# Kernel optimization log

Measured on AMD Instinct MI355X. Metric: run time of the kernel, lower is better.

Reference implementation:

```python
import jax, jax.numpy as jnp
import numpy as np

B, S, E, CS, NC, H = 4, 2048, 1024, 16, 8, 16
D = E + CS            # d_model = 1040
DH = D // H           # head_dim = 65
DFF = 4 * E           # forward_expansion * embed_size


def setup_inputs() -> dict:
    key = jax.random.key(0)
    ks = jax.random.split(key, 20)
    s = 0.02  # init scale for weights
    f32 = jnp.float32
    return {
        'x': jax.random.normal(ks[0], (B, S, E), f32),
        'conditioning': jax.random.uniform(ks[1], (B, S, CS), f32),
        # attention params (torch Linear convention: W is [out, in])
        'Wq': jax.random.normal(ks[2], (D, D), f32) * s,
        'bq': jnp.zeros((D,), f32),
        'Wv': jax.random.normal(ks[3], (D, D), f32) * s,
        'bv': jnp.zeros((D,), f32),
        'Wk': jax.random.normal(ks[4], (NC, D, D), f32) * s,  # stacked per-class key projections
        'bk': jnp.zeros((NC, D), f32),
        'Wo': jax.random.normal(ks[5], (D, D), f32) * s,
        'bo': jnp.zeros((D,), f32),
        # layernorms
        'g1': jnp.ones((E,), f32), 'bn1': jnp.zeros((E,), f32),
        'g2': jnp.ones((E,), f32), 'bn2': jnp.zeros((E,), f32),
        # feed-forward
        'Wf1': jax.random.normal(ks[6], (DFF, E), f32) * s,
        'bf1': jnp.zeros((DFF,), f32),
        'Wf2': jax.random.normal(ks[7], (E, DFF), f32) * s,
        'bf2': jnp.zeros((E,), f32),
    }


def _layernorm(x, g, b, eps=1e-5):
    m = jnp.mean(x, axis=-1, keepdims=True)
    v = jnp.mean(jnp.square(x - m), axis=-1, keepdims=True)
    return (x - m) * jax.lax.rsqrt(v + eps) * g + b


def reference(x, conditioning, Wq, bq, Wv, bv, Wk, bk, Wo, bo,
              g1, bn1, g2, bn2, Wf1, bf1, Wf2, bf2):
    # dropout is identity (eval mode)
    xn = _layernorm(x, g1, bn1)                       # [B,S,E]
    xc = jnp.concatenate([xn, conditioning], axis=-1)  # [B,S,D]

    q = (xc @ Wq.T + bq).reshape(B, S, H, DH).transpose(0, 2, 1, 3)  # [B,H,S,DH]
    v = (xc @ Wv.T + bv).reshape(B, S, H, DH).transpose(0, 2, 1, 3)

    # per-class keys: [B,C,S,D], then weighted-sum by conditioning[:,:,:NC]
    keys = jnp.einsum('bsd,cod->bcso', xc, Wk) + bk[None, :, None, :]
    w = conditioning[:, :, :NC]                        # [B,S,C]
    k = jnp.einsum('bsc,bcso->bso', w, keys)           # [B,S,D]
    k = k.reshape(B, S, H, DH).transpose(0, 2, 1, 3)   # [B,H,S,DH]

    scale = 1.0 / np.sqrt(DH).astype(np.float32)
    scores = jnp.einsum('bhqd,bhkd->bhqk', q, k) * scale
    attn = jax.nn.softmax(scores, axis=-1)
    o = jnp.einsum('bhqk,bhkd->bhqd', attn, v)
    o = o.transpose(0, 2, 1, 3).reshape(B, S, D)
    o = o @ Wo.T + bo

    h = xn + o[:, :, :E]                               # residual uses normed x
    ff = jnp.maximum(h @ Wf1.T + bf1, 0.0) @ Wf2.T + bf2
    return _layernorm(h + ff, g2, bn2)
```

## Files before the change

### kernel.cpp

```cpp
#include <hip/hip_runtime.h>
#include <hip/hip_bf16.h>
#include <math.h>

typedef __bf16 bf16;
typedef __bf16 v8bf __attribute__((ext_vector_type(8)));
typedef float v4f __attribute__((ext_vector_type(4)));

#define B_   4
#define S_   2048
#define E_   1024
#define CS_  16
#define NC_  8
#define H_   16
#define D_   1040
#define DH_  65
#define DFF_ 4096
#define M_   8192
#define KC_  1056
#define KH_  (4 * KC_)
#define KB2_ (8 * KC_)

__device__ __forceinline__ v4f mfma16(v8bf a, v8bf b, v4f c) {
    return __builtin_amdgcn_mfma_f32_16x16x32_bf16(a, b, c, 0, 0, 0);
}

__device__ __forceinline__ void async16(const bf16* g, bf16* l) {
    __builtin_amdgcn_global_load_lds(
        (const __attribute__((address_space(1))) unsigned int*)g,
        (__attribute__((address_space(3))) unsigned int*)l, 16, 0, 0);
}

__global__ __launch_bounds__(256) void k_cvt(const float* __restrict__ src,
                                             bf16* __restrict__ dst, int n) {
    int i = (blockIdx.x * 256 + threadIdx.x) * 4;
    if (i + 4 <= n) {
        float4 v = *(const float4*)(src + i);
        bf16 o[4] = {(bf16)v.x, (bf16)v.y, (bf16)v.z, (bf16)v.w};
        *(ushort4*)(dst + i) = *(const ushort4*)o;
    }
}

__global__ __launch_bounds__(256) void k_build_bk(const float* __restrict__ Wk,
                                                  bf16* __restrict__ Bp) {
    int c = blockIdx.y;
    int idx = blockIdx.x * 256 + threadIdx.x;
    if (idx >= 1040 * 130) return;
    int n = idx / 130, u = idx - n * 130;
    const float* src = Wk + ((size_t)(c * D_ + n)) * D_ + u * 8;
    float4 a = *(const float4*)src;
    float4 b = *(const float4*)(src + 4);
    bf16 o[8] = {(bf16)a.x, (bf16)a.y, (bf16)a.z, (bf16)a.w,
                 (bf16)b.x, (bf16)b.y, (bf16)b.z, (bf16)b.w};
    *(uint4*)(Bp + (size_t)n * KB2_ + c * KC_ + u * 8) = *(const uint4*)o;
}

__global__ __launch_bounds__(256) void k_scale_a(const bf16* __restrict__ xc,
                                                 const float* __restrict__ cond,
                                                 int coff, bf16* __restrict__ Ap) {
    int idx = blockIdx.x * 256 + threadIdx.x;
    int m = idx / 132, u = idx - m * 132;
    int j = u * 8;
    float4 w4 = *(const float4*)(cond + (size_t)m * CS_ + coff);
    float wv[4] = {w4.x, w4.y, w4.z, w4.w};
    bf16* dst = Ap + (size_t)m * KH_ + j;
    if (j < D_) {
        union { uint4 u4; bf16 h[8]; } src;
        src.u4 = *(const uint4*)(xc + (size_t)m * D_ + j);
        float xv[8];
#pragma unroll
        for (int e = 0; e < 8; ++e) xv[e] = (float)src.h[e];
#pragma unroll
        for (int cc = 0; cc < 4; ++cc) {
            bf16 o[8];
#pragma unroll
            for (int e = 0; e < 8; ++e) o[e] = (bf16)(xv[e] * wv[cc]);
            *(uint4*)(dst + cc * KC_) = *(const uint4*)o;
        }
    } else {
        uint4 z = {0u, 0u, 0u, 0u};
#pragma unroll
        for (int cc = 0; cc < 4; ++cc) *(uint4*)(dst + cc * KC_) = z;
    }
}

__global__ __launch_bounds__(256) void k_zero_pads(bf16* __restrict__ qp,
                                                   bf16* __restrict__ kp) {
    int i = blockIdx.x * 256 + threadIdx.x;
    int row = i >> 3, j = i & 7;
    uint4 z = {0u, 0u, 0u, 0u};
    bf16* base = (j < 4) ? qp : kp;
    ((uint4*)(base + (size_t)row * 96 + 64))[j & 3] = z;
}

__global__ __launch_bounds__(256) void k_ln_concat(
    const float* __restrict__ x, const float* __restrict__ cond,
    const float* __restrict__ g, const float* __restrict__ bn,
    bf16* __restrict__ xc)
{
    int row = blockIdx.x;
    int t = threadIdx.x;
    const float* xr = x + (size_t)row * E_;
    float4 v = *(const float4*)(xr + t * 4);
    float s = v.x + v.y + v.z + v.w;
    float ss = v.x * v.x + v.y * v.y + v.z * v.z + v.w * v.w;
#pragma unroll
    for (int off = 32; off; off >>= 1) {
        s  += __shfl_down(s, off);
        ss += __shfl_down(ss, off);
    }
    __shared__ float red[8];
    int wid = t >> 6;
    if ((t & 63) == 0) { red[wid] = s; red[4 + wid] = ss; }
    __syncthreads();
    float stot  = red[0] + red[1] + red[2] + red[3];
    float sstot = red[4] + red[5] + red[6] + red[7];
    float mean = stot * (1.0f / E_);
    float var  = sstot * (1.0f / E_) - mean * mean;
    float rs = rsqrtf(var + 1e-5f);
    bf16* xcr = xc + (size_t)row * D_;
    float vv[4] = {v.x, v.y, v.z, v.w};
#pragma unroll
    for (int j = 0; j < 4; ++j) {
        int i = t * 4 + j;
        xcr[i] = (bf16)(((vv[j] - mean) * rs) * g[i] + bn[i]);
    }
    if (t < CS_) xcr[E_ + t] = (bf16)cond[(size_t)row * CS_ + t];
}

__global__ __launch_bounds__(256) void k_gemm_k2(
    const bf16* __restrict__ A, const bf16* __restrict__ Bm,
    int koffB, bf16* __restrict__ Pout)
{
    __shared__ bf16 As[128][32];
    __shared__ bf16 Bs[128][32];
    int t = threadIdx.x;

    int pid = blockIdx.x;
    int gid = pid / 72;
    int rem = pid - gid * 72;
    int mi = gid * 8 + (rem & 7);
    int ni = rem >> 3;
    int m0 = mi << 7, n0 = ni << 7;

    int lane = t & 63, w = t >> 6;
    int wm = (w >> 1) * 64, wn = (w & 1) * 64;
    int lr = lane & 15, lq = lane >> 4;

    int row_i[2], seg_i[2];
#pragma unroll
    for (int i = 0; i < 2; ++i) { row_i[i] = (t + i * 256) >> 2; seg_i[i] = (t + i * 256) & 3; }

    v4f acc[4][4];
    v4f vzero = {0.f, 0.f, 0.f, 0.f};
#pragma unroll
    for (int mt = 0; mt < 4; ++mt)
#pragma unroll
        for (int nt = 0; nt < 4; ++nt) acc[mt][nt] = vzero;

    for (int kb = 0; kb < KH_ / 32; ++kb) {
        int k0 = kb << 5;
#pragma unroll
        for (int i = 0; i < 2; ++i) {
            async16(A + (size_t)(m0 + row_i[i]) * KH_ + k0 + seg_i[i] * 8,
                    &As[0][0] + (t + i * 256) * 8);
            async16(Bm + (size_t)(n0 + row_i[i]) * KB2_ + koffB + k0 + seg_i[i] * 8,
                    &Bs[0][0] + (t + i * 256) * 8);
        }
        __syncthreads();
        v8bf af[4], bfr[4];
#pragma unroll
        for (int mt = 0; mt < 4; ++mt) af[mt]  = *(const v8bf*)(&As[wm + mt * 16 + lr][lq * 8]);
#pragma unroll
        for (int nt = 0; nt < 4; ++nt) bfr[nt] = *(const v8bf*)(&Bs[wn + nt * 16 + lr][lq * 8]);
#pragma unroll
        for (int mt = 0; mt < 4; ++mt)
#pragma unroll
            for (int nt = 0; nt < 4; ++nt)
                acc[mt][nt] = mfma16(af[mt], bfr[nt], acc[mt][nt]);
        __syncthreads();
    }

#pragma unroll
    for (int mt = 0; mt < 4; ++mt)
#pragma unroll
        for (int reg = 0; reg < 4; ++reg) {
            int grow = m0 + wm + mt * 16 + lq * 4 + reg;
#pragma unroll
            for (int nt = 0; nt < 4; ++nt) {
                int gcol = n0 + wn + nt * 16 + lr;
                if (gcol < D_)
                    Pout[(size_t)grow * D_ + gcol] = (bf16)acc[mt][nt][reg];
            }
        }
}

__global__ __launch_bounds__(256) void k_comb_k(
    const bf16* __restrict__ P0, const bf16* __restrict__ P1,
    const float* __restrict__ condw, const float* __restrict__ bkp,
    bf16* __restrict__ kp)
{
    int idx = blockIdx.x * 256 + threadIdx.x;
    int m = idx / 1040, n = idx - m * 1040;
    float v = (float)P0[idx] + (float)P1[idx];
#pragma unroll
    for (int c = 0; c < NC_; ++c)
        v += condw[(size_t)m * CS_ + c] * bkp[(size_t)c * D_ + n];
    int h = n / 65, d = n - h * 65;
    int b = m >> 11, s = m & 2047;
    int d2 = (d < 64) ? (d ^ ((s & 7) << 3)) : (d ^ ((s & 3) << 3));
    kp[(((size_t)(b * 16 + h)) * S_ + s) * 96 + d2] = (bf16)v;
}

#define EP_QV  0
#define EP_O   1
#define EP_FF1 2
#define EP_FF2 3

template<int EP>
__global__ __launch_bounds__(256) void k_gemm(
    const bf16* __restrict__ A, const bf16* __restrict__ Bm,
    const float* __restrict__ bias, const float* __restrict__ bias2,
    int M, int N, int K, int lda, int ldb, int nbn,
    bf16* __restrict__ Cb, float* __restrict__ Cf, int ldc,
    const bf16* __restrict__ res, int ldres, bf16* __restrict__ Cb2)
{
    __shared__ bf16 As[128][32];
    __shared__ bf16 Bs[128][32];
    int t = threadIdx.x;

    int pid = blockIdx.x;
    int nig = 8 * nbn;
    int gid = pid / nig;
    int rem = pid - gid * nig;
    int mi = gid * 8 + (rem & 7);
    int ni = rem >> 3;
    int m0 = mi << 7, n0 = ni << 7;

    int lane = t & 63, w = t >> 6;
    int wm = (w >> 1) * 64, wn = (w & 1) * 64;
    int lr = lane & 15, lq = lane >> 4;

    int row_i[2], seg_i[2];
#pragma unroll
    for (int i = 0; i < 2; ++i) { row_i[i] = (t + i * 256) >> 2; seg_i[i] = (t + i * 256) & 3; }

    v4f acc[4][4];
    v4f vzero = {0.f, 0.f, 0.f, 0.f};
#pragma unroll
    for (int mt = 0; mt < 4; ++mt)
#pragma unroll
        for (int nt = 0; nt < 4; ++nt) acc[mt][nt] = vzero;

    const int KF = K >> 5;
    const bool KR = (K & 31) != 0;

    for (int kb = 0; kb < KF; ++kb) {
        int k0 = kb << 5;
#pragma unroll
        for (int i = 0; i < 2; ++i) {
            async16(A + (size_t)(m0 + row_i[i]) * lda + k0 + seg_i[i] * 8,
                    &As[0][0] + (t + i * 256) * 8);
            async16(Bm + (size_t)(n0 + row_i[i]) * ldb + k0 + seg_i[i] * 8,
                    &Bs[0][0] + (t + i * 256) * 8);
        }
        __syncthreads();
        v8bf af[4], bfr[4];
#pragma unroll
        for (int mt = 0; mt < 4; ++mt) af[mt]  = *(const v8bf*)(&As[wm + mt * 16 + lr][lq * 8]);
#pragma unroll
        for (int nt = 0; nt < 4; ++nt) bfr[nt] = *(const v8bf*)(&Bs[wn + nt * 16 + lr][lq * 8]);
#pragma unroll
        for (int mt = 0; mt < 4; ++mt)
#pragma unroll
            for (int nt = 0; nt < 4; ++nt)
                acc[mt][nt] = mfma16(af[mt], bfr[nt], acc[mt][nt]);
        __syncthreads();
    }
    if (KR) {
        int k0 = KF << 5;
#pragma unroll
        for (int i = 0; i < 2; ++i) {
            int gk = k0 + seg_i[i] * 8;
            uint4 val = {0u, 0u, 0u, 0u};
            if (gk + 8 <= K) val = *(const uint4*)(A + (size_t)(m0 + row_i[i]) * lda + gk);
            *(uint4*)(&As[row_i[i]][seg_i[i] * 8]) = val;
            uint4 bv = {0u, 0u, 0u, 0u};
            int gn = n0 + row_i[i];
            if (gn < N && gk + 8 <= K) bv = *(const uint4*)(Bm + (size_t)gn * ldb + gk);
            *(uint4*)(&Bs[row_i[i]][seg_i[i] * 8]) = bv;
        }
        __syncthreads();
        v8bf af[4], bfr[4];
#pragma unroll
        for (int mt = 0; mt < 4; ++mt) af[mt]  = *(const v8bf*)(&As[wm + mt * 16 + lr][lq * 8]);
#pragma unroll
        for (int nt = 0; nt < 4; ++nt) bfr[nt] = *(const v8bf*)(&Bs[wn + nt * 16 + lr][lq * 8]);
#pragma unroll
        for (int mt = 0; mt < 4; ++mt)
#pragma unroll
            for (int nt = 0; nt < 4; ++nt)
                acc[mt][nt] = mfma16(af[mt], bfr[nt], acc[mt][nt]);
        __syncthreads();
    }

#pragma unroll
    for (int mt = 0; mt < 4; ++mt) {
#pragma unroll
        for (int reg = 0; reg < 4; ++reg) {
            int grow = m0 + wm + mt * 16 + lq * 4 + reg;
#pragma unroll
            for (int nt = 0; nt < 4; ++nt) {
                int gcol = n0 + wn + nt * 16 + lr;
                float vacc = acc[mt][nt][reg];
                if constexpr (EP == EP_QV) {
                    if (gcol < D_) {
                        float o = (vacc + bias[gcol]) * 0.1789442960f;
                        int h = gcol / 65, d = gcol - h * 65;
                        int b = grow >> 11, s = grow & 2047;
                        Cb[(((size_t)(b * 16 + h)) * S_ + s) * 96 + d] = (bf16)o;
                    } else if (gcol < 2 * D_) {
                        int col = gcol - D_;
                        Cb2[(size_t)grow * D_ + col] = (bf16)(vacc + bias2[col]);
                    }
                } else if constexpr (EP == EP_O) {
                    float o = vacc + bias[gcol] + (float)res[(size_t)grow * ldres + gcol];
                    Cb[(size_t)grow * ldc + gcol] = (bf16)o;
                } else if constexpr (EP == EP_FF1) {
                    float o = vacc + bias[gcol];
                    Cb[(size_t)grow * ldc + gcol] = (bf16)fmaxf(o, 0.f);
                } else {
                    Cf[(size_t)grow * ldc + gcol] =
                        vacc + bias[gcol] + (float)res[(size_t)grow * ldres + gcol];
                }
            }
        }
    }
}

__global__ __launch_bounds__(256) void k_transpose_v(
    const bf16* __restrict__ v, bf16* __restrict__ vt)
{
    int bh = blockIdx.y, s0 = blockIdx.x * 64;
    int b = bh >> 4, h = bh & 15;
    __shared__ bf16 tile[80][65];
#pragma unroll
    for (int i = 0; i < 20; ++i) {
        int idx = threadIdx.x + i * 256;
        int d = idx % 80, sl = idx / 80;
        bf16 val = (bf16)0.f;
        if (d < DH_) val = v[((size_t)b * S_ + s0 + sl) * D_ + h * DH_ + d];
        tile[d][sl] = val;
    }
    __syncthreads();
#pragma unroll
    for (int i = 0; i < 20; ++i) {
        int idx = threadIdx.x + i * 256;
        int sl = idx % 64, d = idx / 64;
        int sl2 = sl ^ ((d & 7) << 3);
        vt[((size_t)bh * 80 + d) * S_ + s0 + sl2] = tile[d][sl];
    }
}

__global__ __launch_bounds__(256) void k_attn(
    const bf16* __restrict__ qp, const bf16* __restrict__ kp,
    const bf16* __restrict__ vt, bf16* __restrict__ o)
{
    int bh = blockIdx.y;
    int s0 = blockIdx.x * 128;
    int b = bh >> 4, h = bh & 15;
    int t = threadIdx.x, lane = t & 63, w = t >> 6;
    int lr = lane & 15, lq = lane >> 4;

    __shared__ bf16 Kbuf[2][64 * 96];
    __shared__ bf16 Vbuf[2][80 * 64];
    __shared__ bf16 Psh[4][16 * 72];
    bf16* Ps = Psh[w];

    v8bf qreg[2][3];
#pragma unroll
    for (int fq = 0; fq < 2; ++fq) {
        const bf16* qbase = qp + ((size_t)bh * S_ + s0 + fq * 64 + w * 16 + lr) * 96;
#pragma unroll
        for (int ks = 0; ks < 3; ++ks)
            qreg[fq][ks] = *(const v8bf*)(qbase + ks * 32 + lq * 8);
    }

    const bf16* kpb = kp + (size_t)bh * S_ * 96;
    const bf16* vpb = vt + (size_t)bh * 80 * S_;

    int vidx[3]; bool vact[3];
#pragma unroll
    for (int i = 0; i < 3; ++i) { vidx[i] = t + i * 256; vact[i] = vidx[i] < 640; }

#pragma unroll
    for (int i = 0; i < 3; ++i)
        async16(kpb + (size_t)(t + i * 256) * 8, &Kbuf[0][(t + i * 256) * 8]);
#pragma unroll
    for (int i = 0; i < 3; ++i)
        if (vact[i])
            async16(vpb + (size_t)(vidx[i] >> 3) * S_ + (vidx[i] & 7) * 8, &Vbuf[0][vidx[i] * 8]);

    float m_0 = -1e30f, l_0 = 0.f, m_1 = -1e30f, l_1 = 0.f;
    v4f oa0[5], oa1[5];
    v4f vzero = {0.f, 0.f, 0.f, 0.f};
#pragma unroll
    for (int nt = 0; nt < 5; ++nt) { oa0[nt] = vzero; oa1[nt] = vzero; }

    int swA = (lr & 7) << 3;
    int swB = (lr & 3) << 3;

    __syncthreads();

    int cur = 0;
    for (int kb = 0; kb < S_ / 64; ++kb) {
        if (kb + 1 < S_ / 64) {
            const bf16* ksrc = kpb + (size_t)(kb + 1) * (64 * 96);
            bf16* Kn = &Kbuf[cur ^ 1][0];
            bf16* Vn = &Vbuf[cur ^ 1][0];
#pragma unroll
            for (int i = 0; i < 3; ++i)
                async16(ksrc + (size_t)(t + i * 256) * 8, Kn + (t + i * 256) * 8);
#pragma unroll
            for (int i = 0; i < 3; ++i)
                if (vact[i])
                    async16(vpb + (size_t)(vidx[i] >> 3) * S_ + (kb + 1) * 64 + (vidx[i] & 7) * 8,
                            Vn + vidx[i] * 8);
        }
        const bf16* Kc = &Kbuf[cur][0];
        const bf16* Vc = &Vbuf[cur][0];

        v4f s0acc[4], s1acc[4];
#pragma unroll
        for (int kt = 0; kt < 4; ++kt) { s0acc[kt] = vzero; s1acc[kt] = vzero; }
        __builtin_amdgcn_s_setprio(1);
#pragma unroll
        for (int ks = 0; ks < 3; ++ks) {
            int cb = (ks * 32 + lq * 8) ^ (ks == 2 ? swB : swA);
#pragma unroll
            for (int kt = 0; kt < 4; ++kt) {
                v8bf kf = *(const v8bf*)(Kc + (kt * 16 + lr) * 96 + cb);
                s0acc[kt] = mfma16(kf, qreg[0][ks], s0acc[kt]);
                s1acc[kt] = mfma16(kf, qreg[1][ks], s1acc[kt]);
            }
        }
        __builtin_amdgcn_s_setprio(0);

        float a0;
        {
            float mx = s0acc[0][0];
#pragma unroll
            for (int kt = 0; kt < 4; ++kt)
#pragma unroll
                for (int r = 0; r < 4; ++r) mx = fmaxf(mx, s0acc[kt][r]);
            mx = fmaxf(mx, __shfl_xor(mx, 16));
            mx = fmaxf(mx, __shfl_xor(mx, 32));
            float mnew = fmaxf(m_0, mx);
            a0 = __builtin_amdgcn_exp2f(m_0 - mnew);
            float ps = 0.f;
#pragma unroll
            for (int kt = 0; kt < 4; ++kt) {
                union { bf16 h[4]; uint2 v; } p4;
#pragma unroll
                for (int r = 0; r < 4; ++r) {
                    float p = __builtin_amdgcn_exp2f(s0acc[kt][r] - mnew);
                    ps += p;
                    p4.h[r] = (bf16)p;
                }
                *(uint2*)(&Ps[lr * 72 + kt * 16 + lq * 4]) = p4.v;
            }
            ps += __shfl_xor(ps, 16);
            ps += __shfl_xor(ps, 32);
            l_0 = l_0 * a0 + ps;
            m_0 = mnew;
        }
        uint2 p1p[4];
        float a1;
        {
            float mx = s1acc[0][0];
#pragma unroll
            for (int kt = 0; kt < 4; ++kt)
#pragma unroll
                for (int r = 0; r < 4; ++r) mx = fmaxf(mx, s1acc[kt][r]);
            mx = fmaxf(mx, __shfl_xor(mx, 16));
            mx = fmaxf(mx, __shfl_xor(mx, 32));
            float mnew = fmaxf(m_1, mx);
            a1 = __builtin_amdgcn_exp2f(m_1 - mnew);
            float ps = 0.f;
#pragma unroll
            for (int kt = 0; kt < 4; ++kt) {
                union { bf16 h[4]; uint2 v; } p4;
#pragma unroll
                for (int r = 0; r < 4; ++r) {
                    float p = __builtin_amdgcn_exp2f(s1acc[kt][r] - mnew);
                    ps += p;
                    p4.h[r] = (bf16)p;
                }
                p1p[kt] = p4.v;
            }
            ps += __shfl_xor(ps, 16);
            ps += __shfl_xor(ps, 32);
            l_1 = l_1 * a1 + ps;
            m_1 = mnew;
        }

        v8bf pf0[2], pf1[2];
        pf0[0] = *(const v8bf*)(&Ps[lr * 72 + lq * 8]);
        pf0[1] = *(const v8bf*)(&Ps[lr * 72 + 32 + lq * 8]);
#pragma unroll
        for (int kt = 0; kt < 4; ++kt)
            *(uint2*)(&Ps[lr * 72 + kt * 16 + lq * 4]) = p1p[kt];
        pf1[0] = *(const v8bf*)(&Ps[lr * 72 + lq * 8]);
        pf1[1] = *(const v8bf*)(&Ps[lr * 72 + 32 + lq * 8]);

#pragma unroll
        for (int nt = 0; nt < 5; ++nt)
#pragma unroll
            for (int r = 0; r < 4; ++r) { oa0[nt][r] *= a0; oa1[nt][r] *= a1; }

        __builtin_amdgcn_s_setprio(1);
#pragma unroll
        for (int kt2 = 0; kt2 < 2; ++kt2) {
            int vb2 = (kt2 * 32 + lq * 8) ^ swA;
#pragma unroll
            for (int nt = 0; nt < 5; ++nt) {
                v8bf vf = *(const v8bf*)(Vc + (nt * 16 + lr) * 64 + vb2);
                oa0[nt] = mfma16(vf, pf0[kt2], oa0[nt]);
                oa1[nt] = mfma16(vf, pf1[kt2], oa1[nt]);
            }
        }
        __builtin_amdgcn_s_setprio(0);
        __syncthreads();
        cur ^= 1;
    }

#pragma unroll
    for (int fq = 0; fq < 2; ++fq) {
        float inv = 1.0f / (fq ? l_1 : l_0);
        const v4f* oa = fq ? oa1 : oa0;
        bf16* obase = o + (size_t)(b * S_ + s0 + fq * 64 + w * 16 + lr) * D_ + h * DH_;
#pragma unroll
        for (int nt = 0; nt < 4; ++nt)
#pragma unroll
            for (int r = 0; r < 4; ++r)
                obase[nt * 16 + lq * 4 + r] = (bf16)(oa[nt][r] * inv);
        if (lq == 0) obase[64] = (bf16)(oa[4][0] * inv);
    }
}

__global__ __launch_bounds__(256) void k_ln_out(
    const float* __restrict__ z, const float* __restrict__ g,
    const float* __restrict__ bn, float* __restrict__ out)
{
    int row = blockIdx.x;
    int t = threadIdx.x;
    const float* zr = z + (size_t)row * E_;
    float4 v = *(const float4*)(zr + t * 4);
    float s = v.x + v.y + v.z + v.w;
    float ss = v.x * v.x + v.y * v.y + v.z * v.z + v.w * v.w;
#pragma unroll
    for (int off = 32; off; off >>= 1) {
        s  += __shfl_down(s, off);
        ss += __shfl_down(ss, off);
    }
    __shared__ float red[8];
    int wid = t >> 6;
    if ((t & 63) == 0) { red[wid] = s; red[4 + wid] = ss; }
    __syncthreads();
    float stot  = red[0] + red[1] + red[2] + red[3];
    float sstot = red[4] + red[5] + red[6] + red[7];
    float mean = stot * (1.0f / E_);
    float var  = sstot * (1.0f / E_) - mean * mean;
    float rs = rsqrtf(var + 1e-5f);
    float* outr = out + (size_t)row * E_;
    float vv[4] = {v.x, v.y, v.z, v.w};
#pragma unroll
    for (int j = 0; j < 4; ++j) {
        int i = t * 4 + j;
        outr[i] = ((vv[j] - mean) * rs) * g[i] + bn[i];
    }
}

extern "C" void kernel_launch(void* const* d_in, const int* in_sizes, int n_in,
                              void* d_out, int out_size, void* d_ws, size_t ws_size,
                              hipStream_t stream) {
    const float* x    = (const float*)d_in[0];
    const float* cond = (const float*)d_in[1];
    const float* Wq   = (const float*)d_in[2];
    const float* bq   = (const float*)d_in[3];
    const float* Wv   = (const float*)d_in[4];
    const float* bv   = (const float*)d_in[5];
    const float* Wk   = (const float*)d_in[6];
    const float* bk   = (const float*)d_in[7];
    const float* Wo   = (const float*)d_in[8];
    const float* bo   = (const float*)d_in[9];
    const float* g1   = (const float*)d_in[10];
    const float* bn1  = (const float*)d_in[11];
    const float* g2   = (const float*)d_in[12];
    const float* bn2  = (const float*)d_in[13];
    const float* Wf1  = (const float*)d_in[14];
    const float* bf1  = (const float*)d_in[15];
    const float* Wf2  = (const float*)d_in[16];
    const float* bf2  = (const float*)d_in[17];
    float* out = (float*)d_out;

    char* ws = (char*)d_ws;
    bf16* Wqv_b = (bf16*)(ws + 0);
    bf16* Wo_b  = (bf16*)(ws + 4526080);
    bf16* Wf1_b = (bf16*)(ws + 6656000);
    bf16* Wf2_b = (bf16*)(ws + 15044608);
    bf16*  xc   = (bf16*)(ws + 23433216);
    bf16*  Bpk  = (bf16*)(ws + 40472576);
    bf16*  Apk  = (bf16*)(ws + 59936768);
    bf16*  P0k  = (bf16*)(ws + 129142784);
    bf16*  P1k  = (bf16*)(ws + 146182144);
    bf16*  qp   = (bf16*)(ws + 40472576);
    bf16*  kp   = (bf16*)(ws + 65638400);
    bf16*  vb   = (bf16*)(ws + 90804224);
    bf16*  hb   = (bf16*)(ws + 90804224);
    bf16*  vtb  = (bf16*)(ws + 107843584);
    bf16*  ob   = (bf16*)(ws + 128815104);
    bf16*  ff1  = (bf16*)(ws + 23433216);
    float* zb   = (float*)(ws + 107843584);

    k_cvt<<<(1081600 / 4 + 255) / 256, 256, 0, stream>>>(Wq, Wqv_b, 1081600);
    k_cvt<<<(1081600 / 4 + 255) / 256, 256, 0, stream>>>(Wv, Wqv_b + 1081600, 1081600);
    k_cvt<<<(1064960 / 4 + 255) / 256, 256, 0, stream>>>(Wo, Wo_b, 1064960);
    k_cvt<<<(4194304 / 4 + 255) / 256, 256, 0, stream>>>(Wf1, Wf1_b, 4194304);
    k_cvt<<<(4194304 / 4 + 255) / 256, 256, 0, stream>>>(Wf2, Wf2_b, 4194304);

    k_ln_concat<<<M_, 256, 0, stream>>>(x, cond, g1, bn1, xc);

    k_build_bk<<<dim3((1040 * 130 + 255) / 256, 8), 256, 0, stream>>>(Wk, Bpk);
    k_scale_a<<<(M_ * 132) / 256, 256, 0, stream>>>(xc, cond, 0, Apk);
    k_gemm_k2<<<576, 256, 0, stream>>>(Apk, Bpk, 0, P0k);
    k_scale_a<<<(M_ * 132) / 256, 256, 0, stream>>>(xc, cond, 4, Apk);
    k_gemm_k2<<<576, 256, 0, stream>>>(Apk, Bpk, KH_, P1k);

    k_zero_pads<<<4096, 256, 0, stream>>>(qp, kp);
    k_comb_k<<<(M_ * D_) / 256, 256, 0, stream>>>(P0k, P1k, cond, bk, kp);

    k_gemm<EP_QV><<<64 * 17, 256, 0, stream>>>(xc, Wqv_b, bq, bv, M_, 2 * D_, D_, D_, D_, 17,
                                               qp, nullptr, 0, nullptr, 0, vb);

    k_transpose_v<<<dim3(S_ / 64, 64), 256, 0, stream>>>(vb, vtb);
    k_attn<<<dim3(S_ / 128, 64), 256, 0, stream>>>(qp, kp, vtb, ob);

    k_gemm<EP_O><<<64 * 8, 256, 0, stream>>>(ob, Wo_b, bo, nullptr, M_, E_, D_, D_, D_, 8,
                                             hb, nullptr, E_, xc, D_, nullptr);
    k_gemm<EP_FF1><<<64 * 32, 256, 0, stream>>>(hb, Wf1_b, bf1, nullptr, M_, DFF_, E_, E_, E_, 32,
                                                ff1, nullptr, DFF_, nullptr, 0, nullptr);
    k_gemm<EP_FF2><<<64 * 8, 256, 0, stream>>>(ff1, Wf2_b, bf2, nullptr, M_, E_, DFF_, DFF_, DFF_, 8,
                                               nullptr, zb, E_, hb, E_, nullptr);

    k_ln_out<<<M_, 256, 0, stream>>>(zb, g2, bn2, out);
}
```

Before: 958.9 us.

## Lazy softmax rescaling, MFMA row-sum via ones column, and XCD-aware block swizzle

The attention kernel now skips the running-max update and accumulator rescale unless some row's max grows by more than 8 (in log2 units), and drops the explicit per-block row-sum shuffles. Instead it places a column of ones in the padded V tile, so the PV MFMA produces the softmax denominator as a by-product. GEMM and attention block indices are also remapped so neighbouring tiles land on the same XCD for L2 reuse. This trades exact per-block max tracking for bounded exponent growth (risking bf16 precision loss in P), and adds a wave-wide vote per block.

```diff
diff --git a/kernel.cpp b/kernel.cpp
--- a/kernel.cpp
+++ b/kernel.cpp
@@ -30,6 +30,11 @@
         (__attribute__((address_space(3))) unsigned int*)l, 16, 0, 0);
 }
 
+__device__ __forceinline__ int xcd_swz(int pid, int nwg) {
+    int cpx = nwg >> 3;
+    return (pid & 7) * cpx + (pid >> 3);
+}
+
 __global__ __launch_bounds__(256) void k_cvt(const float* __restrict__ src,
                                              bf16* __restrict__ dst, int n) {
     int i = (blockIdx.x * 256 + threadIdx.x) * 4;
@@ -135,7 +140,7 @@
     __shared__ bf16 Bs[128][32];
     int t = threadIdx.x;
 
-    int pid = blockIdx.x;
+    int pid = xcd_swz(blockIdx.x, gridDim.x);
     int gid = pid / 72;
     int rem = pid - gid * 72;
     int mi = gid * 8 + (rem & 7);
@@ -228,7 +233,7 @@
     __shared__ bf16 Bs[128][32];
     int t = threadIdx.x;
 
-    int pid = blockIdx.x;
+    int pid = xcd_swz(blockIdx.x, gridDim.x);
     int nig = 8 * nbn;
     int gid = pid / nig;
     int rem = pid - gid * nig;
@@ -349,6 +354,7 @@
         int d = idx % 80, sl = idx / 80;
         bf16 val = (bf16)0.f;
         if (d < DH_) val = v[((size_t)b * S_ + s0 + sl) * D_ + h * DH_ + d];
+        else if (d == DH_) val = (bf16)1.0f;
         tile[d][sl] = val;
     }
     __syncthreads();
@@ -365,8 +371,10 @@
     const bf16* __restrict__ qp, const bf16* __restrict__ kp,
     const bf16* __restrict__ vt, bf16* __restrict__ o)
 {
-    int bh = blockIdx.y;
-    int s0 = blockIdx.x * 128;
+    int wgid = blockIdx.y * gridDim.x + blockIdx.x;
+    int g = wgid & 7, ii = wgid >> 3;
+    int bh = g * 8 + (ii >> 4);
+    int s0 = (ii & 15) * 128;
     int b = bh >> 4, h = bh & 15;
     int t = threadIdx.x, lane = t & 63, w = t >> 6;
     int lr = lane & 15, lq = lane >> 4;
@@ -400,7 +408,7 @@
         if (vact[i])
             async16(vpb + (size_t)(vidx[i] >> 3) * S_ + (vidx[i] & 7) * 8, &Vbuf[0][vidx[i] * 8]);
 
-    float m_0 = -1e30f, l_0 = 0.f, m_1 = -1e30f, l_1 = 0.f;
+    float m_0 = -1e30f, m_1 = -1e30f;
     v4f oa0[5], oa1[5];
     v4f vzero = {0.f, 0.f, 0.f, 0.f};
 #pragma unroll
@@ -445,62 +453,58 @@
         }
         __builtin_amdgcn_s_setprio(0);
 
-        float a0;
         {
-            float mx = s0acc[0][0];
+            float pmax = s0acc[0][0];
 #pragma unroll
             for (int kt = 0; kt < 4; ++kt)
 #pragma unroll
-                for (int r = 0; r < 4; ++r) mx = fmaxf(mx, s0acc[kt][r]);
-            mx = fmaxf(mx, __shfl_xor(mx, 16));
-            mx = fmaxf(mx, __shfl_xor(mx, 32));
-            float mnew = fmaxf(m_0, mx);
-            a0 = __builtin_amdgcn_exp2f(m_0 - mnew);
-            float ps = 0.f;
+                for (int r = 0; r < 4; ++r) pmax = fmaxf(pmax, s0acc[kt][r]);
+            if (!__all(pmax - m_0 <= 8.0f)) {
+                float mx = fmaxf(pmax, __shfl_xor(pmax, 16));
+                mx = fmaxf(mx, __shfl_xor(mx, 32));
+                float mnew = fmaxf(m_0, mx);
+                float a0 = __builtin_amdgcn_exp2f(m_0 - mnew);
+#pragma unroll
+                for (int nt = 0; nt < 5; ++nt)
+#pragma unroll
+                    for (int r = 0; r < 4; ++r) oa0[nt][r] *= a0;
+                m_0 = mnew;
+            }
 #pragma unroll
             for (int kt = 0; kt < 4; ++kt) {
                 union { bf16 h[4]; uint2 v; } p4;
 #pragma unroll
-                for (int r = 0; r < 4; ++r) {
-                    float p = __builtin_amdgcn_exp2f(s0acc[kt][r] - mnew);
-                    ps += p;
-                    p4.h[r] = (bf16)p;
-                }
+                for (int r = 0; r < 4; ++r)
+                    p4.h[r] = (bf16)__builtin_amdgcn_exp2f(s0acc[kt][r] - m_0);
                 *(uint2*)(&Ps[lr * 72 + kt * 16 + lq * 4]) = p4.v;
             }
-            ps += __shfl_xor(ps, 16);
-            ps += __shfl_xor(ps, 32);
-            l_0 = l_0 * a0 + ps;
-            m_0 = mnew;
         }
         uint2 p1p[4];
-        float a1;
         {
-            float mx = s1acc[0][0];
+            float pmax = s1acc[0][0];
 #pragma unroll
             for (int kt = 0; kt < 4; ++kt)
 #pragma unroll
-                for (int r = 0; r < 4; ++r) mx = fmaxf(mx, s1acc[kt][r]);
-            mx = fmaxf(mx, __shfl_xor(mx, 16));
-            mx = fmaxf(mx, __shfl_xor(mx, 32));
-            float mnew = fmaxf(m_1, mx);
-            a1 = __builtin_amdgcn_exp2f(m_1 - mnew);
-            float ps = 0.f;
+                for (int r = 0; r < 4; ++r) pmax = fmaxf(pmax, s1acc[kt][r]);
+            if (!__all(pmax - m_1 <= 8.0f)) {
+                float mx = fmaxf(pmax, __shfl_xor(pmax, 16));
+                mx = fmaxf(mx, __shfl_xor(mx, 32));
+                float mnew = fmaxf(m_1, mx);
+                float a1 = __builtin_amdgcn_exp2f(m_1 - mnew);
+#pragma unroll
+                for (int nt = 0; nt < 5; ++nt)
+#pragma unroll
+                    for (int r = 0; r < 4; ++r) oa1[nt][r] *= a1;
+                m_1 = mnew;
+            }
 #pragma unroll
             for (int kt = 0; kt < 4; ++kt) {
                 union { bf16 h[4]; uint2 v; } p4;
 #pragma unroll
-                for (int r = 0; r < 4; ++r) {
-                    float p = __builtin_amdgcn_exp2f(s1acc[kt][r] - mnew);
-                    ps += p;
-                    p4.h[r] = (bf16)p;
-                }
+                for (int r = 0; r < 4; ++r)
+                    p4.h[r] = (bf16)__builtin_amdgcn_exp2f(s1acc[kt][r] - m_1);
                 p1p[kt] = p4.v;
             }
-            ps += __shfl_xor(ps, 16);
-            ps += __shfl_xor(ps, 32);
-            l_1 = l_1 * a1 + ps;
-            m_1 = mnew;
         }
 
         v8bf pf0[2], pf1[2];
@@ -512,11 +516,6 @@
         pf1[0] = *(const v8bf*)(&Ps[lr * 72 + lq * 8]);
         pf1[1] = *(const v8bf*)(&Ps[lr * 72 + 32 + lq * 8]);
 
-#pragma unroll
-        for (int nt = 0; nt < 5; ++nt)
-#pragma unroll
-            for (int r = 0; r < 4; ++r) { oa0[nt][r] *= a0; oa1[nt][r] *= a1; }
-
         __builtin_amdgcn_s_setprio(1);
 #pragma unroll
         for (int kt2 = 0; kt2 < 2; ++kt2) {
@@ -533,9 +532,12 @@
         cur ^= 1;
     }
 
+    float l0v = __shfl(oa0[4][1], lr);
+    float l1v = __shfl(oa1[4][1], lr);
+
 #pragma unroll
     for (int fq = 0; fq < 2; ++fq) {
-        float inv = 1.0f / (fq ? l_1 : l_0);
+        float inv = 1.0f / (fq ? l1v : l0v);
         const v4f* oa = fq ? oa1 : oa0;
         bf16* obase = o + (size_t)(b * S_ + s0 + fq * 64 + w * 16 + lr) * D_ + h * DH_;
 #pragma unroll
```

After: 932.0 us. -2.8%, faster.
